# Optimization experiments

Hardware: AMD Instinct MI355X
Metric: run time of the kernel (lower is better)

## Reference

```python
import jax, jax.numpy as jnp
import numpy as np

ALPHA = 0.25
GAMMA = 2.0
COST_MASK = 1.0
COST_DICE = 1.0


def setup_inputs() -> dict:
    key = jax.random.key(0)
    k1, k2 = jax.random.split(key)
    B, N, M, H, W = 4, 100, 20, 256, 256
    outputs = jax.random.normal(k1, (B, N, H, W), dtype=jnp.float32)
    # binary target masks; threshold ensures every mask is non-empty so the
    # data-dependent tgt_ids truncation in the original is a no-op
    targets = (jax.random.uniform(k2, (B, M, H, W)) > 0.7).astype(jnp.float32)
    return {"outputs": outputs, "targets": targets}


def _cost_matrix(out_mask, tgt_mask):
    # out_mask: [N, HW] logits, tgt_mask: [M, HW] binary
    hw = out_mask.shape[1]
    prob = jax.nn.sigmoid(out_mask)
    # BCE-with-logits: target=1 -> softplus(-x); target=0 -> softplus(x)
    bce_pos = jax.nn.softplus(-out_mask)
    bce_neg = jax.nn.softplus(out_mask)
    focal_pos = ALPHA * (1.0 - prob) ** GAMMA * bce_pos            # [N, HW]
    focal_neg = (1.0 - ALPHA) * prob ** GAMMA * bce_neg            # [N, HW]
    cost_mask = (jnp.einsum('nc,mc->nm', focal_pos, tgt_mask)
                 + jnp.einsum('nc,mc->nm', focal_neg, 1.0 - tgt_mask)) / hw
    # dice cost
    numerator = 2.0 * jnp.einsum('nc,mc->nm', prob, tgt_mask)
    denominator = prob.sum(-1)[:, None] + tgt_mask.sum(-1)[None, :]
    cost_dice = 1.0 - (numerator + 1.0) / (denominator + 1.0)
    return COST_MASK * cost_mask + COST_DICE * cost_dice           # [N, M]


def reference(outputs, targets):
    B, N, H, W = outputs.shape
    M = targets.shape[1]
    out_flat = outputs.reshape(B, N, H * W)
    tgt_flat = targets.reshape(B, M, H * W)
    # vmap over batch: per-image [N, M] cost matrix fed to Hungarian on CPU
    C = jax.vmap(_cost_matrix)(out_flat, tgt_flat)  # [B, N, M]
    return C
```

## Files before the change

### kernel.cpp

```cpp
#include <hip/hip_runtime.h>
#include <math.h>

#define BB 4
#define NN 100
#define MM 20
#define HWPIX 65536
#define NT 7
#define GSEG 64
#define BLKPX (HWPIX / GSEG)
#define WAVEPX 256
#define NCHUNK (WAVEPX / 32)
#define PSLOTS 728

typedef float f32x4 __attribute__((ext_vector_type(4)));
typedef short bf16x8 __attribute__((ext_vector_type(8)));

__global__ __launch_bounds__(256) void pack_kernel(
    const float* __restrict__ tgt,
    unsigned int* __restrict__ masks)
{
    const int b = blockIdx.x >> 6;
    const int c = ((blockIdx.x & 63) << 10) | (threadIdx.x << 2);
    const float* tb = tgt + (size_t)b * MM * HWPIX + c;

    unsigned int mk0 = 0, mk1 = 0, mk2 = 0, mk3 = 0;
#pragma unroll
    for (int m = 0; m < MM; ++m) {
        const f32x4 t = *(const f32x4*)(tb + (size_t)m * HWPIX);
        mk0 |= (t.x > 0.5f) ? (1u << m) : 0u;
        mk1 |= (t.y > 0.5f) ? (1u << m) : 0u;
        mk2 |= (t.z > 0.5f) ? (1u << m) : 0u;
        mk3 |= (t.w > 0.5f) ? (1u << m) : 0u;
    }
    uint4 v; v.x = mk0; v.y = mk1; v.z = mk2; v.w = mk3;
    *(uint4*)(masks + (size_t)b * HWPIX + c) = v;
}

__global__ __launch_bounds__(256, 4) void cost_mfma_kernel(
    const float* __restrict__ out,
    const unsigned int* __restrict__ masks,
    float* __restrict__ part)
{
    const int g    = blockIdx.x & (GSEG - 1);
    const int nt   = (blockIdx.x >> 6) % NT;
    const int b    = blockIdx.x / (GSEG * NT);
    const int tid  = threadIdx.x;
    const int w    = tid >> 6;
    const int lane = tid & 63;
    const int lrow = lane & 15;
    const int quad = lane >> 4;

    const int n = min(nt * 16 + lrow, NN - 1);
    const float* xrow        = out + (size_t)(b * NN + n) * HWPIX;
    const unsigned int* mrow = masks + (size_t)b * HWPIX;

    const int kw = g * BLKPX + w * WAVEPX + quad * 8;

    f32x4 d1a = {0,0,0,0}, d1b = {0,0,0,0};
    f32x4 d2a = {0,0,0,0}, d2b = {0,0,0,0};
    f32x4 d3a = {0,0,0,0}, d3b = {0,0,0,0};
    float sfn = 0.f, sp = 0.f;

    bf16x8 ones;
#pragma unroll
    for (int j = 0; j < 8; ++j) ones[j] = (short)0x3F80;

#define EVALJ(XV, MK, J)                                                    \
    {                                                                       \
        const float x_   = (XV);                                            \
        const float ex_  = __builtin_amdgcn_exp2f(x_ * 1.44269504f);        \
        const float ope_ = 1.f + ex_;                                       \
        const float bn_  = 0.69314718f * __builtin_amdgcn_logf(ope_);       \
        const float bp_  = bn_ - x_;                                        \
        const float p_   = ex_ * __builtin_amdgcn_rcpf(ope_);               \
        const float om_  = 1.f - p_;                                        \
        const float fpv_ = (0.25f * om_) * (om_ * bp_);                     \
        const float fnv_ = (0.75f * p_) * (p_ * bn_);                       \
        sfn += fnv_; sp += p_;                                              \
        fdv[J] = (short)__builtin_bit_cast(unsigned short, (__bf16)(fpv_ - fnv_)); \
        fpr[J] = (short)__builtin_bit_cast(unsigned short, (__bf16)p_);     \
        const unsigned s_ = (MK) >> lrow;                                   \
        t0[J]  = (short)((s_ & 1u) * 0x3F80u);                              \
        t1[J]  = (short)(((s_ >> 16) & 1u) * 0x3F80u);                      \
    }

    f32x4 xaC = *(const f32x4*)(xrow + kw);
    f32x4 xbC = *(const f32x4*)(xrow + kw + 4);
    uint4 qaC = *(const uint4*)(mrow + kw);
    uint4 qbC = *(const uint4*)(mrow + kw + 4);

#pragma unroll
    for (int ch = 0; ch < NCHUNK; ++ch) {
        f32x4 xaN, xbN; uint4 qaN, qbN;
        if (ch < NCHUNK - 1) {
            const int k1 = kw + (ch + 1) * 32;
            xaN = *(const f32x4*)(xrow + k1);
            xbN = *(const f32x4*)(xrow + k1 + 4);
            qaN = *(const uint4*)(mrow + k1);
            qbN = *(const uint4*)(mrow + k1 + 4);
        }

        bf16x8 fdv, fpr, t0, t1;
        EVALJ(xaC.x, qaC.x, 0)
        EVALJ(xaC.y, qaC.y, 1)
        EVALJ(xaC.z, qaC.z, 2)
        EVALJ(xaC.w, qaC.w, 3)
        EVALJ(xbC.x, qbC.x, 4)
        EVALJ(xbC.y, qbC.y, 5)
        EVALJ(xbC.z, qbC.z, 6)
        EVALJ(xbC.w, qbC.w, 7)

        d1a = __builtin_amdgcn_mfma_f32_16x16x32_bf16(fdv,  t0, d1a, 0, 0, 0);
        d2a = __builtin_amdgcn_mfma_f32_16x16x32_bf16(fpr,  t0, d2a, 0, 0, 0);
        d3a = __builtin_amdgcn_mfma_f32_16x16x32_bf16(ones, t0, d3a, 0, 0, 0);
        d1b = __builtin_amdgcn_mfma_f32_16x16x32_bf16(fdv,  t1, d1b, 0, 0, 0);
        d2b = __builtin_amdgcn_mfma_f32_16x16x32_bf16(fpr,  t1, d2b, 0, 0, 0);
        d3b = __builtin_amdgcn_mfma_f32_16x16x32_bf16(ones, t1, d3b, 0, 0, 0);

        if (ch < NCHUNK - 1) {
            xaC = xaN; xbC = xbN; qaC = qaN; qbC = qbN;
        }
    }
#undef EVALJ

    sfn += __shfl_xor(sfn, 16, 64); sfn += __shfl_xor(sfn, 32, 64);
    sp  += __shfl_xor(sp,  16, 64); sp  += __shfl_xor(sp,  32, 64);

    __shared__ float lds[4 * PSLOTS];
    float* lw = lds + w * PSLOTS;
#pragma unroll
    for (int r = 0; r < 4; ++r) {
        const int nl = quad * 4 + r;
        lw[nl * 44 + lrow]      = d1a[r];
        lw[nl * 44 + 20 + lrow] = d2a[r];
        if (lrow < 4) {
            lw[nl * 44 + 16 + lrow] = d1b[r];
            lw[nl * 44 + 36 + lrow] = d2b[r];
        }
    }
    if (lane < 16) {
        lw[lrow * 44 + 40] = sfn;
        lw[lrow * 44 + 41] = sp;
        lw[lrow * 44 + 42] = 0.f;
        lw[lrow * 44 + 43] = 0.f;
    }
    if (quad == 0) {
        lw[704 + lrow] = d3a[0];
        if (lrow < 4) lw[720 + lrow] = d3b[0];
    }
    if (quad == 1 && lrow < 4) lw[724 + lrow] = 0.f;
    __syncthreads();

    float* pout = part + (size_t)blockIdx.x * PSLOTS;
    for (int idx = tid; idx < PSLOTS; idx += 256)
        pout[idx] = lds[idx] + lds[PSLOTS + idx] + lds[2 * PSLOTS + idx]
                  + lds[3 * PSLOTS + idx];
}

__global__ __launch_bounds__(256) void combine_kernel(
    const float* __restrict__ part,
    float* __restrict__ C)
{
    const int bn = blockIdx.x;
    const int b  = bn / NN;
    const int n  = bn - b * NN;
    const int nt = n >> 4, nl = n & 15;
    const float* pbase = part + (size_t)((b * NT + nt) * GSEG) * PSLOTS;

    const int t  = threadIdx.x;
    const int s  = t & 63;
    const int gp = t >> 6;

    float acc = 0.f;
    if (s < 44) {
        const int off = nl * 44 + s;
#pragma unroll
        for (int gg = 0; gg < 16; ++gg)
            acc += pbase[(size_t)(gp * 16 + gg) * PSLOTS + off];
    } else {
        const int off = 704 + (s - 44);
#pragma unroll
        for (int gg = 0; gg < 16; ++gg)
            acc += pbase[(size_t)(gp * 16 + gg) * PSLOTS + off];
    }

    __shared__ float r1[4][64];
    r1[gp][s] = acc;
    __syncthreads();

    if (t < MM) {
        const int m = t;
        float D1 = 0.f, D2 = 0.f, SFN = 0.f, SP = 0.f, TS = 0.f;
#pragma unroll
        for (int g4 = 0; g4 < 4; ++g4) {
            D1  += r1[g4][m];
            D2  += r1[g4][20 + m];
            SFN += r1[g4][40];
            SP  += r1[g4][41];
            TS  += r1[g4][44 + m];
        }
        const float cost_mask = (SFN + D1) * (1.f / (float)HWPIX);
        const float den  = SP + TS;
        const float dice = 1.f - (2.f * D2 + 1.f) / (den + 1.f);
        C[bn * MM + m] = cost_mask + dice;
    }
}

extern "C" void kernel_launch(void* const* d_in, const int* in_sizes, int n_in,
                              void* d_out, int out_size, void* d_ws, size_t ws_size,
                              hipStream_t stream)
{
    const float* outp = (const float*)d_in[0];
    const float* tgtp = (const float*)d_in[1];
    float* C = (float*)d_out;

    char* ws = (char*)d_ws;
    unsigned int* masks = (unsigned int*)ws;
    float* part = (float*)(ws + (size_t)BB * HWPIX * sizeof(unsigned int));

    pack_kernel<<<BB * 64, 256, 0, stream>>>(tgtp, masks);
    cost_mfma_kernel<<<BB * NT * GSEG, 256, 0, stream>>>(outp, masks, part);
    combine_kernel<<<BB * NN, 256, 0, stream>>>(part, C);
}
```

Measured before the change: 177.5 us.

## Stage logits through LDS with coalesced global_load_lds row loads

Replaces the strided per-lane register loads of logits (each lane reading 8 floats from its own row) with rounds in which each wave uses global_load_lds to copy whole contiguous 256-pixel row segments into a padded LDS tile. Compute then reads the tile back from LDS. The aim is fully coalesced global reads. In exchange it drops the register double-buffered prefetch and adds two block barriers per round, which limits overlap of load and compute. The LDS buffer is shared with the epilogue, sized 16*260 floats against the 4*728 slots it must hold.

```diff
diff --git a/kernel.cpp b/kernel.cpp
--- a/kernel.cpp
+++ b/kernel.cpp
@@ -8,8 +8,8 @@
 #define NT 7
 #define GSEG 64
 #define BLKPX (HWPIX / GSEG)
-#define WAVEPX 256
-#define NCHUNK (WAVEPX / 32)
+#define ROUNDPX 256
+#define LDSROW 260
 #define PSLOTS 728
 
 typedef float f32x4 __attribute__((ext_vector_type(4)));
@@ -50,11 +50,10 @@
     const int lrow = lane & 15;
     const int quad = lane >> 4;
 
-    const int n = min(nt * 16 + lrow, NN - 1);
-    const float* xrow        = out + (size_t)(b * NN + n) * HWPIX;
+    __shared__ __align__(16) float lds[16 * LDSROW];
+
     const unsigned int* mrow = masks + (size_t)b * HWPIX;
-
-    const int kw = g * BLKPX + w * WAVEPX + quad * 8;
+    const int colbase = g * BLKPX;
 
     f32x4 d1a = {0,0,0,0}, d1b = {0,0,0,0};
     f32x4 d2a = {0,0,0,0}, d2b = {0,0,0,0};
@@ -75,7 +74,7 @@
         const float p_   = ex_ * __builtin_amdgcn_rcpf(ope_);               \
         const float om_  = 1.f - p_;                                        \
         const float fpv_ = (0.25f * om_) * (om_ * bp_);                     \
-        const float fnv_ = (0.75f * p_) * (p_ * bn_);                       \
+        const float fnv_ = (0.75f * p_) * (p_ * bn_);                      \
         sfn += fnv_; sp += p_;                                              \
         fdv[J] = (short)__builtin_bit_cast(unsigned short, (__bf16)(fpv_ - fnv_)); \
         fpr[J] = (short)__builtin_bit_cast(unsigned short, (__bf16)p_);     \
@@ -84,49 +83,51 @@
         t1[J]  = (short)(((s_ >> 16) & 1u) * 0x3F80u);                      \
     }
 
-    f32x4 xaC = *(const f32x4*)(xrow + kw);
-    f32x4 xbC = *(const f32x4*)(xrow + kw + 4);
-    uint4 qaC = *(const uint4*)(mrow + kw);
-    uint4 qbC = *(const uint4*)(mrow + kw + 4);
-
-#pragma unroll
-    for (int ch = 0; ch < NCHUNK; ++ch) {
-        f32x4 xaN, xbN; uint4 qaN, qbN;
-        if (ch < NCHUNK - 1) {
-            const int k1 = kw + (ch + 1) * 32;
-            xaN = *(const f32x4*)(xrow + k1);
-            xbN = *(const f32x4*)(xrow + k1 + 4);
-            qaN = *(const uint4*)(mrow + k1);
-            qbN = *(const uint4*)(mrow + k1 + 4);
-        }
-
-        bf16x8 fdv, fpr, t0, t1;
-        EVALJ(xaC.x, qaC.x, 0)
-        EVALJ(xaC.y, qaC.y, 1)
-        EVALJ(xaC.z, qaC.z, 2)
-        EVALJ(xaC.w, qaC.w, 3)
-        EVALJ(xbC.x, qbC.x, 4)
-        EVALJ(xbC.y, qbC.y, 5)
-        EVALJ(xbC.z, qbC.z, 6)
-        EVALJ(xbC.w, qbC.w, 7)
-
-        d1a = __builtin_amdgcn_mfma_f32_16x16x32_bf16(fdv,  t0, d1a, 0, 0, 0);
-        d2a = __builtin_amdgcn_mfma_f32_16x16x32_bf16(fpr,  t0, d2a, 0, 0, 0);
-        d3a = __builtin_amdgcn_mfma_f32_16x16x32_bf16(ones, t0, d3a, 0, 0, 0);
-        d1b = __builtin_amdgcn_mfma_f32_16x16x32_bf16(fdv,  t1, d1b, 0, 0, 0);
-        d2b = __builtin_amdgcn_mfma_f32_16x16x32_bf16(fpr,  t1, d2b, 0, 0, 0);
-        d3b = __builtin_amdgcn_mfma_f32_16x16x32_bf16(ones, t1, d3b, 0, 0, 0);
-
-        if (ch < NCHUNK - 1) {
-            xaC = xaN; xbC = xbN; qaC = qaN; qbC = qbN;
-        }
+    for (int r = 0; r < 4; ++r) {
+#pragma unroll
+        for (int rr = 0; rr < 4; ++rr) {
+            const int rs = w * 4 + rr;
+            const int gn = min(nt * 16 + rs, NN - 1);
+            const float* gp = out + (size_t)(b * NN + gn) * HWPIX
+                            + colbase + r * ROUNDPX + lane * 4;
+            __builtin_amdgcn_global_load_lds(gp, &lds[rs * LDSROW], 16, 0, 0);
+        }
+        __syncthreads();
+
+#pragma unroll
+        for (int c = 0; c < 2; ++c) {
+            const int lcol = w * 64 + c * 32 + quad * 8;
+            const float* xp = &lds[lrow * LDSROW + lcol];
+            const f32x4 xaC = *(const f32x4*)xp;
+            const f32x4 xbC = *(const f32x4*)(xp + 4);
+            const unsigned* mp = mrow + colbase + r * ROUNDPX + lcol;
+            const uint4 qaC = *(const uint4*)mp;
+            const uint4 qbC = *(const uint4*)(mp + 4);
+
+            bf16x8 fdv, fpr, t0, t1;
+            EVALJ(xaC.x, qaC.x, 0)
+            EVALJ(xaC.y, qaC.y, 1)
+            EVALJ(xaC.z, qaC.z, 2)
+            EVALJ(xaC.w, qaC.w, 3)
+            EVALJ(xbC.x, qbC.x, 4)
+            EVALJ(xbC.y, qbC.y, 5)
+            EVALJ(xbC.z, qbC.z, 6)
+            EVALJ(xbC.w, qbC.w, 7)
+
+            d1a = __builtin_amdgcn_mfma_f32_16x16x32_bf16(fdv,  t0, d1a, 0, 0, 0);
+            d2a = __builtin_amdgcn_mfma_f32_16x16x32_bf16(fpr,  t0, d2a, 0, 0, 0);
+            d3a = __builtin_amdgcn_mfma_f32_16x16x32_bf16(ones, t0, d3a, 0, 0, 0);
+            d1b = __builtin_amdgcn_mfma_f32_16x16x32_bf16(fdv,  t1, d1b, 0, 0, 0);
+            d2b = __builtin_amdgcn_mfma_f32_16x16x32_bf16(fpr,  t1, d2b, 0, 0, 0);
+            d3b = __builtin_amdgcn_mfma_f32_16x16x32_bf16(ones, t1, d3b, 0, 0, 0);
+        }
+        __syncthreads();
     }
 #undef EVALJ
 
     sfn += __shfl_xor(sfn, 16, 64); sfn += __shfl_xor(sfn, 32, 64);
     sp  += __shfl_xor(sp,  16, 64); sp  += __shfl_xor(sp,  32, 64);
 
-    __shared__ float lds[4 * PSLOTS];
     float* lw = lds + w * PSLOTS;
 #pragma unroll
     for (int r = 0; r < 4; ++r) {
```

New measurement: 177.4 us. Within noise of the previous version (-0.1%).
